# Kernel tuning notes

Hardware: AMD Instinct MI355X
Metric: run time of the kernel (lower is better)

## Reference

```python
import jax, jax.numpy as jnp
import numpy as np

K = 1024       # num_embeddings
D = 64         # embedding_dim
DECAY = 0.99
COMMIT = 0.25
EPS = 1e-05


def setup_inputs() -> dict:
    key = jax.random.key(0)
    k1, k2, k3 = jax.random.split(key, 3)
    x = jax.random.normal(k1, (16, 64, 64, 64), jnp.float32)  # NCHW, C == D
    embedding_weight = jax.random.normal(k2, (K, D), jnp.float32)
    ema_weight = jax.random.normal(k3, (K, D), jnp.float32)
    ema_cluster_size = jnp.zeros((K,), jnp.float32)
    return {"x": x, "embedding_weight": embedding_weight,
            "ema_cluster_size": ema_cluster_size, "ema_weight": ema_weight}


def reference(x, embedding_weight, ema_cluster_size, ema_weight):
    # NCHW -> NHWC, flatten tokens
    xp = jnp.transpose(x, (0, 2, 3, 1))            # [B,H,W,D]
    flat = xp.reshape(-1, D)                        # [N,D]
    dists = ((flat ** 2).sum(1, keepdims=True)
             + (embedding_weight ** 2).sum(1)
             - 2.0 * flat @ embedding_weight.T)     # [N,K]
    idx = jnp.argmin(dists, axis=1)                 # [N]
    encodings = jax.nn.one_hot(idx, K, dtype=flat.dtype)  # [N,K]
    quantized = jnp.take(embedding_weight, idx, axis=0).reshape(xp.shape)
    # training-mode EMA updates (scatter-add instead of dense one-hot matmuls)
    counts = jnp.zeros((K,), flat.dtype).at[idx].add(1.0)
    new_cs = ema_cluster_size * DECAY + (1.0 - DECAY) * counts
    n = new_cs.sum()
    new_cs = (new_cs + EPS) / (n + K * EPS) * n     # Laplace smoothing
    dw = jnp.zeros((K, D), flat.dtype).at[idx].add(flat)
    new_ema_weight = ema_weight * DECAY + (1.0 - DECAY) * dw
    new_embedding = new_ema_weight / new_cs[:, None]
    # commitment loss and straight-through estimator
    e_latent_loss = jnp.mean((jax.lax.stop_gradient(quantized) - xp) ** 2)
    loss = COMMIT * e_latent_loss
    q_st = xp + jax.lax.stop_gradient(quantized - xp)
    return (loss, jnp.transpose(q_st, (0, 3, 1, 2)), encodings,
            new_embedding, new_cs, new_ema_weight)
```

## Files before the change

kernel.cpp:

```cpp
#include <hip/hip_runtime.h>

#define HW 4096
#define DECAYF 0.99f
#define ONEMF 0.01f
#define EPSF 1e-5f
#define BIAS 192.0f

typedef __bf16 bf16x8 __attribute__((ext_vector_type(8)));
typedef float f32x4 __attribute__((ext_vector_type(4)));
typedef unsigned short ushort8 __attribute__((ext_vector_type(8)));

#define WS_DW     0
#define WS_COUNTS 1048576
#define WS_NCHALF 1064960
#define WS_SSE    1065984
#define WS_IDX    1066000
#define WS_EHI    1131536
#define WS_ELO    1164304

__device__ __forceinline__ float wave_reduce_add(float v) {
#pragma unroll
    for (int o = 32; o > 0; o >>= 1) v += __shfl_xor(v, o, 64);
    return v;
}

__device__ __forceinline__ unsigned short bf_rne(float f) {
    unsigned int u = __float_as_uint(f);
    unsigned int r = u + 0x7fffu + ((u >> 16) & 1u);
    return (unsigned short)(r >> 16);
}

__device__ __forceinline__ unsigned med3u(unsigned a, unsigned b, unsigned c) {
    unsigned mn = a < b ? a : b;
    unsigned mx = a > b ? a : b;
    unsigned t = mx < c ? mx : c;
    return mn > t ? mn : t;
}

__global__ __launch_bounds__(256) void prep_kernel(const float* __restrict__ E,
                                                   float* __restrict__ ws) {
    const int bid = blockIdx.x, tid = threadIdx.x;
    const int id = bid * 256 + tid;
    ws[id] = 0.0f;
    if (bid == 0 && tid == 0) ws[WS_SSE] = 0.0f;
    if (bid < 256) {
        const float v = E[id];
        const unsigned short h = bf_rne(v);
        const float hf = __uint_as_float((unsigned int)h << 16);
        const unsigned short l = bf_rne(v - hf);
        ((unsigned short*)(ws + WS_EHI))[id] = h;
        ((unsigned short*)(ws + WS_ELO))[id] = l;
        const float s = wave_reduce_add(v * v);
        if ((tid & 63) == 0) ws[WS_NCHALF + (id >> 6)] = -0.5f * s;
    }
}

__global__ __launch_bounds__(256) void vq_main(const float* __restrict__ x,
                                               const float* __restrict__ E,
                                               float* __restrict__ out,
                                               float* __restrict__ ws) {
    const int tid = threadIdx.x;
    const int lane = tid & 63;
    const int w = tid >> 6;
    const int q = lane >> 4, m = lane & 15;
    const int blk = blockIdx.x;
    const int bb = blk >> 5;
    const int hw0 = (blk & 31) << 7;
    const int tok0 = blk << 7;

    __shared__ float xs[128 * 68];
    __shared__ unsigned t1s[4][32][16], t2s[4][32][16];
    __shared__ int idx_sh[128];

    {
        const float* xb = x + ((size_t)bb << 18) + hw0;
#pragma unroll
        for (int cc = 0; cc < 32; ++cc) {
            const int id = cc * 256 + tid;
            const int c = id >> 7, t = id & 127;
            xs[t * 68 + c] = xb[((size_t)c << 12) + t];
        }
    }
    __syncthreads();

    bf16x8 Ah[2][2], Al[2][2];
#pragma unroll
    for (int t = 0; t < 2; ++t) {
        const int tok = w * 32 + t * 16 + m;
#pragma unroll
        for (int s = 0; s < 2; ++s) {
            const float* p = &xs[tok * 68 + s * 32 + q * 8];
            ushort8 hu, lu;
#pragma unroll
            for (int j = 0; j < 8; ++j) {
                const float f = p[j];
                const unsigned short h = bf_rne(f);
                const float hf = __uint_as_float((unsigned int)h << 16);
                hu[j] = h;
                lu[j] = bf_rne(f - hf);
            }
            Ah[t][s] = __builtin_bit_cast(bf16x8, hu);
            Al[t][s] = __builtin_bit_cast(bf16x8, lu);
        }
    }

    const ushort8* __restrict__ Ehp = (const ushort8*)(ws + WS_EHI);
    const ushort8* __restrict__ Elp = (const ushort8*)(ws + WS_ELO);
    const float* __restrict__ ncp = ws + WS_NCHALF;

    unsigned b1[2][4] = {{0,0,0,0},{0,0,0,0}}, b2[2][4] = {{0,0,0,0},{0,0,0,0}};

    ushort8 nb0h = Ehp[m * 8 + q];
    ushort8 nb1h = Ehp[m * 8 + 4 + q];
    ushort8 nb0l = Elp[m * 8 + q];
    ushort8 nb1l = Elp[m * 8 + 4 + q];
    float nnc = ncp[m];

    for (int ck = 0; ck < 64; ++ck) {
        const ushort8 c0h = nb0h, c1h = nb1h, c0l = nb0l, c1l = nb1l;
        const float nc = nnc;
        if (ck < 63) {
            const int code = (ck + 1) * 16 + m;
            nb0h = Ehp[code * 8 + q];
            nb1h = Ehp[code * 8 + 4 + q];
            nb0l = Elp[code * 8 + q];
            nb1l = Elp[code * 8 + 4 + q];
            nnc = ncp[code];
        }
        const bf16x8 bh0 = __builtin_bit_cast(bf16x8, c0h);
        const bf16x8 bh1 = __builtin_bit_cast(bf16x8, c1h);
        const bf16x8 bl0 = __builtin_bit_cast(bf16x8, c0l);
        const bf16x8 bl1 = __builtin_bit_cast(bf16x8, c1l);
        const float base = nc + BIAS;
#pragma unroll
        for (int t = 0; t < 2; ++t) {
            f32x4 acc = {base, base, base, base};
            acc = __builtin_amdgcn_mfma_f32_16x16x32_bf16(Ah[t][0], bh0, acc, 0, 0, 0);
            acc = __builtin_amdgcn_mfma_f32_16x16x32_bf16(Ah[t][1], bh1, acc, 0, 0, 0);
            acc = __builtin_amdgcn_mfma_f32_16x16x32_bf16(Al[t][0], bh0, acc, 0, 0, 0);
            acc = __builtin_amdgcn_mfma_f32_16x16x32_bf16(Al[t][1], bh1, acc, 0, 0, 0);
            acc = __builtin_amdgcn_mfma_f32_16x16x32_bf16(Ah[t][0], bl0, acc, 0, 0, 0);
            acc = __builtin_amdgcn_mfma_f32_16x16x32_bf16(Ah[t][1], bl1, acc, 0, 0, 0);
#pragma unroll
            for (int r = 0; r < 4; ++r) {
                const unsigned p = (__float_as_uint(acc[r]) & ~63u) | (unsigned)ck;
                b2[t][r] = med3u(b1[t][r], b2[t][r], p);
                b1[t][r] = b1[t][r] > p ? b1[t][r] : p;
            }
        }
    }

#pragma unroll
    for (int t = 0; t < 2; ++t)
#pragma unroll
        for (int r = 0; r < 4; ++r) {
            t1s[w][t * 16 + q * 4 + r][m] = b1[t][r];
            t2s[w][t * 16 + q * 4 + r][m] = b2[t][r];
        }

    float dval = 0.0f;
    if (lane < 32) {
        unsigned s1 = 0, s2 = 0;
        int c1 = 0, c2 = 0;
#pragma unroll 4
        for (int mm = 0; mm < 16; ++mm) {
            const unsigned a = t1s[w][lane][mm];
            const int codeA = (int)((a & 63u) << 4) | mm;
            if (a > s1) { s2 = s1; c2 = c1; s1 = a; c1 = codeA; }
            else if (a > s2) { s2 = a; c2 = codeA; }
            const unsigned bsec = t2s[w][lane][mm];
            if (bsec > s2) { s2 = bsec; c2 = (int)((bsec & 63u) << 4) | mm; }
        }
        const int tokL = w * 32 + lane;
        const int ca = c1 < c2 ? c1 : c2;
        const int cb = c1 < c2 ? c2 : c1;
        const f32x4* Ea4 = (const f32x4*)(E + ca * 64);
        const f32x4* Eb4 = (const f32x4*)(E + cb * 64);
        const f32x4* xr4 = (const f32x4*)(&xs[tokL * 68]);
        double sa = 0, ea = 0, sb = 0, eb = 0, x2 = 0;
#pragma unroll 4
        for (int c4 = 0; c4 < 16; ++c4) {
            const f32x4 ev = Ea4[c4], fv = Eb4[c4], xv4 = xr4[c4];
#pragma unroll
            for (int j = 0; j < 4; ++j) {
                const double xv = (double)xv4[j];
                const double va = (double)ev[j], vb = (double)fv[j];
                sa += xv * va; ea += va * va;
                sb += xv * vb; eb += vb * vb;
                x2 += xv * xv;
            }
        }
        const double qa = ea - 2.0 * sa;
        const double qb = eb - 2.0 * sb;
        int best; double qq;
        if (qb < qa) { best = cb; qq = qb; } else { best = ca; qq = qa; }
        idx_sh[tokL] = best;
        ((int*)(ws + WS_IDX))[tok0 + tokL] = best;
        float dd = (float)(qq + x2);
        dval = dd < 0.f ? 0.f : dd;
        atomicAdd(&ws[WS_COUNTS + (blk & 15) * 1024 + best], 1.0f);
    }
    const float ssum = wave_reduce_add(dval);
    if (lane == 0) atomicAdd(&ws[WS_SSE], ssum);
    __syncthreads();

    float* outq = out + 1;
#pragma unroll
    for (int cc = 0; cc < 32; ++cc) {
        const int id = cc * 256 + tid;
        const int c = id >> 7, t = id & 127;
        const int kb = idx_sh[t];
        const float xv = xs[t * 68 + c];
        const float eq = E[kb * 64 + c];
        outq[((size_t)(bb * 64 + c) << 12) + hw0 + t] = xv + (eq - xv);
    }
    {
        float* dwr = ws + WS_DW + (size_t)(blk & 15) * 65536;
#pragma unroll 4
        for (int tt = 0; tt < 32; ++tt) {
            const int t = w * 32 + tt;
            const int kb = idx_sh[t];
            atomicAdd(&dwr[kb * 64 + lane], xs[t * 68 + lane]);
        }
    }
}

__global__ __launch_bounds__(256) void enc_write(const float* __restrict__ ws,
                                                 float* __restrict__ out) {
    const int tid = threadIdx.x;
    const int c0 = tid << 2;
    const int row0 = blockIdx.x << 5;
    const int* __restrict__ idxp = (const int*)(ws + WS_IDX);
    float* enc = out + 1 + (size_t)4194304;
    for (int r = 0; r < 32; ++r) {
        const int row = row0 + r;
        const int kb = idxp[row];
        f32x4 v;
        v[0] = (c0 == kb) ? 1.0f : 0.0f;
        v[1] = (c0 + 1 == kb) ? 1.0f : 0.0f;
        v[2] = (c0 + 2 == kb) ? 1.0f : 0.0f;
        v[3] = (c0 + 3 == kb) ? 1.0f : 0.0f;
        *(f32x4*)(enc + (size_t)row * 1024 + c0) = v;
    }
}

__global__ __launch_bounds__(1024) void fin_cs(const float* __restrict__ cs_in,
                                               float* __restrict__ out,
                                               const float* __restrict__ ws) {
    __shared__ float red[16];
    __shared__ float n_sh;
    const int tid = threadIdx.x;
    float cnt = 0.f;
#pragma unroll
    for (int p = 0; p < 16; ++p) cnt += ws[WS_COUNTS + p * 1024 + tid];
    const float raw = cs_in[tid] * DECAYF + ONEMF * cnt;
    const float s = wave_reduce_add(raw);
    if ((tid & 63) == 0) red[tid >> 6] = s;
    __syncthreads();
    if (tid == 0) {
        float n = 0.f;
#pragma unroll
        for (int i = 0; i < 16; ++i) n += red[i];
        n_sh = n;
        out[0] = 0.25f * ws[WS_SSE] * (1.0f / 4194304.0f);
    }
    __syncthreads();
    const float n = n_sh;
    out[71368705 + tid] = (raw + EPSF) / (n + 1024.0f * EPSF) * n;
}

__global__ __launch_bounds__(256) void fin_w(const float* __restrict__ emaw,
                                             float* __restrict__ out,
                                             const float* __restrict__ ws) {
    const int i = blockIdx.x * 256 + threadIdx.x;
    float acc = 0.f;
#pragma unroll
    for (int p = 0; p < 16; ++p) acc += ws[WS_DW + p * 65536 + i];
    const float val = emaw[i] * DECAYF + ONEMF * acc;
    out[71369729 + i] = val;
    const float cs = out[71368705 + (i >> 6)];
    out[71303169 + i] = val / cs;
}

extern "C" void kernel_launch(void* const* d_in, const int* in_sizes, int n_in,
                              void* d_out, int out_size, void* d_ws, size_t ws_size,
                              hipStream_t stream) {
    const float* x    = (const float*)d_in[0];
    const float* E    = (const float*)d_in[1];
    const float* cs   = (const float*)d_in[2];
    const float* emaw = (const float*)d_in[3];
    float* out = (float*)d_out;
    float* ws  = (float*)d_ws;

    prep_kernel<<<4160, 256, 0, stream>>>(E, ws);
    vq_main<<<512, 256, 0, stream>>>(x, E, out, ws);
    enc_write<<<2048, 256, 0, stream>>>(ws, out);
    fin_cs<<<1, 1024, 0, stream>>>(cs, out, ws);
    fin_w<<<256, 256, 0, stream>>>(emaw, out, ws);
}
```

Before: 422.9 us.

## Split codebook scan across two wave groups and reduce top-2 via shuffles

Doubles the vq_main block to 512 threads so each token tile's codebook scan is split between two halves of 32 code chunks each. The inner loop now keeps two prefetch streams in flight. The per-lane top-2 merge is moved into cross-lane shuffles before the shared-memory exchange. This aims to double the waves per CU on a 512-block grid, which otherwise underfills the GPU, and to shorten the serial scan. The cost is more registers, extra shuffle and shared-memory traffic, and a final merge done by only half the waves.

New measurement: 419.0 us. No clear change (-0.9%).

```diff
diff --git a/kernel.cpp b/kernel.cpp
--- a/kernel.cpp
+++ b/kernel.cpp
@@ -55,13 +55,15 @@
     }
 }
 
-__global__ __launch_bounds__(256) void vq_main(const float* __restrict__ x,
-                                               const float* __restrict__ E,
-                                               float* __restrict__ out,
-                                               float* __restrict__ ws) {
+__global__ __launch_bounds__(512, 4) void vq_main(const float* __restrict__ x,
+                                                  const float* __restrict__ E,
+                                                  float* __restrict__ out,
+                                                  float* __restrict__ ws) {
     const int tid = threadIdx.x;
     const int lane = tid & 63;
     const int w = tid >> 6;
+    const int wg = w & 3;
+    const int kh = w >> 2;
     const int q = lane >> 4, m = lane & 15;
     const int blk = blockIdx.x;
     const int bb = blk >> 5;
@@ -69,14 +71,15 @@
     const int tok0 = blk << 7;
 
     __shared__ float xs[128 * 68];
-    __shared__ unsigned t1s[4][32][16], t2s[4][32][16];
+    __shared__ unsigned t1s[8][32][4], t2s[8][32][4];
+    __shared__ int t1c[8][32][4], t2c[8][32][4];
     __shared__ int idx_sh[128];
 
     {
         const float* xb = x + ((size_t)bb << 18) + hw0;
 #pragma unroll
-        for (int cc = 0; cc < 32; ++cc) {
-            const int id = cc * 256 + tid;
+        for (int cc = 0; cc < 16; ++cc) {
+            const int id = cc * 512 + tid;
             const int c = id >> 7, t = id & 127;
             xs[t * 68 + c] = xb[((size_t)c << 12) + t];
         }
@@ -86,7 +89,7 @@
     bf16x8 Ah[2][2], Al[2][2];
 #pragma unroll
     for (int t = 0; t < 2; ++t) {
-        const int tok = w * 32 + t * 16 + m;
+        const int tok = wg * 32 + t * 16 + m;
 #pragma unroll
         for (int s = 0; s < 2; ++s) {
             const float* p = &xs[tok * 68 + s * 32 + q * 8];
@@ -110,27 +113,21 @@
 
     unsigned b1[2][4] = {{0,0,0,0},{0,0,0,0}}, b2[2][4] = {{0,0,0,0},{0,0,0,0}};
 
-    ushort8 nb0h = Ehp[m * 8 + q];
-    ushort8 nb1h = Ehp[m * 8 + 4 + q];
-    ushort8 nb0l = Elp[m * 8 + q];
-    ushort8 nb1l = Elp[m * 8 + 4 + q];
-    float nnc = ncp[m];
-
-    for (int ck = 0; ck < 64; ++ck) {
-        const ushort8 c0h = nb0h, c1h = nb1h, c0l = nb0l, c1l = nb1l;
-        const float nc = nnc;
-        if (ck < 63) {
-            const int code = (ck + 1) * 16 + m;
-            nb0h = Ehp[code * 8 + q];
-            nb1h = Ehp[code * 8 + 4 + q];
-            nb0l = Elp[code * 8 + q];
-            nb1l = Elp[code * 8 + 4 + q];
-            nnc = ncp[code];
-        }
-        const bf16x8 bh0 = __builtin_bit_cast(bf16x8, c0h);
-        const bf16x8 bh1 = __builtin_bit_cast(bf16x8, c1h);
-        const bf16x8 bl0 = __builtin_bit_cast(bf16x8, c0l);
-        const bf16x8 bl1 = __builtin_bit_cast(bf16x8, c1l);
+    const int ck0 = kh * 32;
+    const int codeA0 = ck0 * 16 + m, codeB0 = (ck0 + 1) * 16 + m;
+    ushort8 hA0 = Ehp[codeA0 * 8 + q],     hA1 = Ehp[codeA0 * 8 + 4 + q];
+    ushort8 lA0 = Elp[codeA0 * 8 + q],     lA1 = Elp[codeA0 * 8 + 4 + q];
+    float   ncA = ncp[codeA0];
+    ushort8 hB0 = Ehp[codeB0 * 8 + q],     hB1 = Ehp[codeB0 * 8 + 4 + q];
+    ushort8 lB0 = Elp[codeB0 * 8 + q],     lB1 = Elp[codeB0 * 8 + 4 + q];
+    float   ncB = ncp[codeB0];
+
+    auto compute = [&](const ushort8& h0, const ushort8& h1, const ushort8& l0,
+                       const ushort8& l1, float nc, int ckv) {
+        const bf16x8 bh0 = __builtin_bit_cast(bf16x8, h0);
+        const bf16x8 bh1 = __builtin_bit_cast(bf16x8, h1);
+        const bf16x8 bl0 = __builtin_bit_cast(bf16x8, l0);
+        const bf16x8 bl1 = __builtin_bit_cast(bf16x8, l1);
         const float base = nc + BIAS;
 #pragma unroll
         for (int t = 0; t < 2; ++t) {
@@ -143,71 +140,129 @@
             acc = __builtin_amdgcn_mfma_f32_16x16x32_bf16(Ah[t][1], bl1, acc, 0, 0, 0);
 #pragma unroll
             for (int r = 0; r < 4; ++r) {
-                const unsigned p = (__float_as_uint(acc[r]) & ~63u) | (unsigned)ck;
+                const unsigned p = (__float_as_uint(acc[r]) & ~63u) | (unsigned)ckv;
                 b2[t][r] = med3u(b1[t][r], b2[t][r], p);
                 b1[t][r] = b1[t][r] > p ? b1[t][r] : p;
             }
         }
-    }
-
+    };
+
+    for (int j2 = 0; j2 < 16; ++j2) {
+        const int ckA = ck0 + 2 * j2;
+        const ushort8 ch0 = hA0, ch1 = hA1, cl0 = lA0, cl1 = lA1; const float cnc = ncA;
+        {
+            const int nc_ = (j2 < 15) ? (ckA + 2) * 16 + m : codeA0;
+            hA0 = Ehp[nc_ * 8 + q]; hA1 = Ehp[nc_ * 8 + 4 + q];
+            lA0 = Elp[nc_ * 8 + q]; lA1 = Elp[nc_ * 8 + 4 + q];
+            ncA = ncp[nc_];
+        }
+        compute(ch0, ch1, cl0, cl1, cnc, ckA);
+        const ushort8 dh0 = hB0, dh1 = hB1, dl0 = lB0, dl1 = lB1; const float dnc = ncB;
+        {
+            const int nc_ = (j2 < 15) ? (ckA + 3) * 16 + m : codeB0;
+            hB0 = Ehp[nc_ * 8 + q]; hB1 = Ehp[nc_ * 8 + 4 + q];
+            lB0 = Elp[nc_ * 8 + q]; lB1 = Elp[nc_ * 8 + 4 + q];
+            ncB = ncp[nc_];
+        }
+        compute(dh0, dh1, dl0, dl1, dnc, ckA + 1);
+    }
+
+    int c1[2][4], c2[2][4];
 #pragma unroll
     for (int t = 0; t < 2; ++t)
 #pragma unroll
         for (int r = 0; r < 4; ++r) {
-            t1s[w][t * 16 + q * 4 + r][m] = b1[t][r];
-            t2s[w][t * 16 + q * 4 + r][m] = b2[t][r];
-        }
+            c1[t][r] = (int)((b1[t][r] & 63u) << 4) | m;
+            c2[t][r] = (int)((b2[t][r] & 63u) << 4) | m;
+        }
+#pragma unroll
+    for (int d = 1; d < 4; d <<= 1) {
+#pragma unroll
+        for (int t = 0; t < 2; ++t)
+#pragma unroll
+            for (int r = 0; r < 4; ++r) {
+                const unsigned o1 = __shfl_xor(b1[t][r], d, 64);
+                const int      oc1 = __shfl_xor(c1[t][r], d, 64);
+                const unsigned o2 = __shfl_xor(b2[t][r], d, 64);
+                const int      oc2 = __shfl_xor(c2[t][r], d, 64);
+                const bool win = o1 > b1[t][r];
+                const unsigned n1 = win ? o1 : b1[t][r]; const int nc1 = win ? oc1 : c1[t][r];
+                const unsigned ls = win ? b1[t][r] : o1; const int lc = win ? c1[t][r] : oc1;
+                const unsigned os = win ? o2 : b2[t][r]; const int oc = win ? oc2 : c2[t][r];
+                const bool sec = ls > os;
+                b1[t][r] = n1; c1[t][r] = nc1;
+                b2[t][r] = sec ? ls : os; c2[t][r] = sec ? lc : oc;
+            }
+    }
+    if ((m & 3) == 0) {
+        const int g = m >> 2;
+#pragma unroll
+        for (int t = 0; t < 2; ++t)
+#pragma unroll
+            for (int r = 0; r < 4; ++r) {
+                const int trow = t * 16 + q * 4 + r;
+                t1s[w][trow][g] = b1[t][r]; t1c[w][trow][g] = c1[t][r];
+                t2s[w][trow][g] = b2[t][r]; t2c[w][trow][g] = c2[t][r];
+            }
+    }
+    __syncthreads();
 
     float dval = 0.0f;
-    if (lane < 32) {
-        unsigned s1 = 0, s2 = 0;
-        int c1 = 0, c2 = 0;
+    if (w < 4) {
+        if (lane < 32) {
+            const int trow = lane;
+            unsigned s1 = 0, s2 = 0;
+            int cc1 = 0, cc2 = 0;
+#pragma unroll
+            for (int h = 0; h < 2; ++h) {
+                const int ww = wg + h * 4;
+#pragma unroll
+                for (int g = 0; g < 4; ++g) {
+                    const unsigned a = t1s[ww][trow][g]; const int ac = t1c[ww][trow][g];
+                    if (a > s1) { s2 = s1; cc2 = cc1; s1 = a; cc1 = ac; }
+                    else if (a > s2) { s2 = a; cc2 = ac; }
+                    const unsigned bs = t2s[ww][trow][g]; const int bc = t2c[ww][trow][g];
+                    if (bs > s2) { s2 = bs; cc2 = bc; }
+                }
+            }
+            const int tokL = wg * 32 + lane;
+            const int ca = cc1 < cc2 ? cc1 : cc2;
+            const int cb = cc1 < cc2 ? cc2 : cc1;
+            const f32x4* Ea4 = (const f32x4*)(E + ca * 64);
+            const f32x4* Eb4 = (const f32x4*)(E + cb * 64);
+            const f32x4* xr4 = (const f32x4*)(&xs[tokL * 68]);
+            double sa = 0, ea = 0, sb = 0, eb = 0, x2 = 0;
 #pragma unroll 4
-        for (int mm = 0; mm < 16; ++mm) {
-            const unsigned a = t1s[w][lane][mm];
-            const int codeA = (int)((a & 63u) << 4) | mm;
-            if (a > s1) { s2 = s1; c2 = c1; s1 = a; c1 = codeA; }
-            else if (a > s2) { s2 = a; c2 = codeA; }
-            const unsigned bsec = t2s[w][lane][mm];
-            if (bsec > s2) { s2 = bsec; c2 = (int)((bsec & 63u) << 4) | mm; }
-        }
-        const int tokL = w * 32 + lane;
-        const int ca = c1 < c2 ? c1 : c2;
-        const int cb = c1 < c2 ? c2 : c1;
-        const f32x4* Ea4 = (const f32x4*)(E + ca * 64);
-        const f32x4* Eb4 = (const f32x4*)(E + cb * 64);
-        const f32x4* xr4 = (const f32x4*)(&xs[tokL * 68]);
-        double sa = 0, ea = 0, sb = 0, eb = 0, x2 = 0;
-#pragma unroll 4
-        for (int c4 = 0; c4 < 16; ++c4) {
-            const f32x4 ev = Ea4[c4], fv = Eb4[c4], xv4 = xr4[c4];
-#pragma unroll
-            for (int j = 0; j < 4; ++j) {
-                const double xv = (double)xv4[j];
-                const double va = (double)ev[j], vb = (double)fv[j];
-                sa += xv * va; ea += va * va;
-                sb += xv * vb; eb += vb * vb;
-                x2 += xv * xv;
-            }
-        }
-        const double qa = ea - 2.0 * sa;
-        const double qb = eb - 2.0 * sb;
-        int best; double qq;
-        if (qb < qa) { best = cb; qq = qb; } else { best = ca; qq = qa; }
-        idx_sh[tokL] = best;
-        ((int*)(ws + WS_IDX))[tok0 + tokL] = best;
-        float dd = (float)(qq + x2);
-        dval = dd < 0.f ? 0.f : dd;
-        atomicAdd(&ws[WS_COUNTS + (blk & 15) * 1024 + best], 1.0f);
-    }
-    const float ssum = wave_reduce_add(dval);
-    if (lane == 0) atomicAdd(&ws[WS_SSE], ssum);
+            for (int c4 = 0; c4 < 16; ++c4) {
+                const f32x4 ev = Ea4[c4], fv = Eb4[c4], xv4 = xr4[c4];
+#pragma unroll
+                for (int j = 0; j < 4; ++j) {
+                    const double xv = (double)xv4[j];
+                    const double va = (double)ev[j], vb = (double)fv[j];
+                    sa += xv * va; ea += va * va;
+                    sb += xv * vb; eb += vb * vb;
+                    x2 += xv * xv;
+                }
+            }
+            const double qa = ea - 2.0 * sa;
+            const double qb = eb - 2.0 * sb;
+            int best; double qq;
+            if (qb < qa) { best = cb; qq = qb; } else { best = ca; qq = qa; }
+            idx_sh[tokL] = best;
+            ((int*)(ws + WS_IDX))[tok0 + tokL] = best;
+            float dd = (float)(qq + x2);
+            dval = dd < 0.f ? 0.f : dd;
+            atomicAdd(&ws[WS_COUNTS + (blk & 15) * 1024 + best], 1.0f);
+        }
+        const float ssum = wave_reduce_add(dval);
+        if (lane == 0) atomicAdd(&ws[WS_SSE], ssum);
+    }
     __syncthreads();
 
     float* outq = out + 1;
 #pragma unroll
-    for (int cc = 0; cc < 32; ++cc) {
-        const int id = cc * 256 + tid;
+    for (int cc = 0; cc < 16; ++cc) {
+        const int id = cc * 512 + tid;
         const int c = id >> 7, t = id & 127;
         const int kb = idx_sh[t];
         const float xv = xs[t * 68 + c];
@@ -217,8 +272,8 @@
     {
         float* dwr = ws + WS_DW + (size_t)(blk & 15) * 65536;
 #pragma unroll 4
-        for (int tt = 0; tt < 32; ++tt) {
-            const int t = w * 32 + tt;
+        for (int tt = 0; tt < 16; ++tt) {
+            const int t = w * 16 + tt;
             const int kb = idx_sh[t];
             atomicAdd(&dwr[kb * 64 + lane], xs[t * 68 + lane]);
         }
@@ -293,7 +348,7 @@
     float* ws  = (float*)d_ws;
 
     prep_kernel<<<4160, 256, 0, stream>>>(E, ws);
-    vq_main<<<512, 256, 0, stream>>>(x, E, out, ws);
+    vq_main<<<512, 512, 0, stream>>>(x, E, out, ws);
     enc_write<<<2048, 256, 0, stream>>>(ws, out);
     fin_cs<<<1, 1024, 0, stream>>>(cs, out, ws);
     fin_w<<<256, 256, 0, stream>>>(emaw, out, ws);
```

## Split VQ search into codebook-panel kernel, top-2 merge, and output pass

Applied to the files above, without the earlier changes.

The single 512-block search kernel becomes a 4096-block kernel where each block handles 128 tokens against a 128-code panel, staged in LDS. Each block writes per-panel top-2 candidates to workspace, and a separate merge kernel picks the final index with a double-precision recheck. The quantized output and dw scatter move into their own kernel, and workspace zeroing uses hipMemsetAsync. The intent is more parallelism and occupancy across the device, paid for with extra launches, extra global traffic for top-2 candidates, and re-reading x several times.

Result: slower. 439.6 us (+3.9%).

```diff
diff --git a/kernel.cpp b/kernel.cpp
--- a/kernel.cpp
+++ b/kernel.cpp
@@ -1,10 +1,8 @@
 #include <hip/hip_runtime.h>
 
-#define HW 4096
 #define DECAYF 0.99f
 #define ONEMF 0.01f
 #define EPSF 1e-5f
-#define BIAS 192.0f
 
 typedef __bf16 bf16x8 __attribute__((ext_vector_type(8)));
 typedef float f32x4 __attribute__((ext_vector_type(4)));
@@ -17,6 +15,7 @@
 #define WS_IDX    1066000
 #define WS_EHI    1131536
 #define WS_ELO    1164304
+#define WS_TOP2   1197072
 
 __device__ __forceinline__ float wave_reduce_add(float v) {
 #pragma unroll
@@ -30,198 +29,247 @@
     return (unsigned short)(r >> 16);
 }
 
-__device__ __forceinline__ unsigned med3u(unsigned a, unsigned b, unsigned c) {
-    unsigned mn = a < b ? a : b;
-    unsigned mx = a > b ? a : b;
-    unsigned t = mx < c ? mx : c;
-    return mn > t ? mn : t;
-}
-
 __global__ __launch_bounds__(256) void prep_kernel(const float* __restrict__ E,
                                                    float* __restrict__ ws) {
-    const int bid = blockIdx.x, tid = threadIdx.x;
-    const int id = bid * 256 + tid;
-    ws[id] = 0.0f;
-    if (bid == 0 && tid == 0) ws[WS_SSE] = 0.0f;
-    if (bid < 256) {
-        const float v = E[id];
-        const unsigned short h = bf_rne(v);
-        const float hf = __uint_as_float((unsigned int)h << 16);
-        const unsigned short l = bf_rne(v - hf);
-        ((unsigned short*)(ws + WS_EHI))[id] = h;
-        ((unsigned short*)(ws + WS_ELO))[id] = l;
-        const float s = wave_reduce_add(v * v);
-        if ((tid & 63) == 0) ws[WS_NCHALF + (id >> 6)] = -0.5f * s;
-    }
-}
-
-__global__ __launch_bounds__(256) void vq_main(const float* __restrict__ x,
-                                               const float* __restrict__ E,
-                                               float* __restrict__ out,
-                                               float* __restrict__ ws) {
+    const int id = blockIdx.x * 256 + threadIdx.x;
+    const float v = E[id];
+    const unsigned short h = bf_rne(v);
+    const float hf = __uint_as_float((unsigned int)h << 16);
+    const unsigned short l = bf_rne(v - hf);
+    ((unsigned short*)(ws + WS_EHI))[id] = h;
+    ((unsigned short*)(ws + WS_ELO))[id] = l;
+    const float s = wave_reduce_add(v * v);
+    if ((threadIdx.x & 63) == 0) ws[WS_NCHALF + (id >> 6)] = -0.5f * s;
+}
+
+__global__ __launch_bounds__(256, 2) void vq_panel(const float* __restrict__ x,
+                                                   float* __restrict__ ws) {
     const int tid = threadIdx.x;
     const int lane = tid & 63;
     const int w = tid >> 6;
     const int q = lane >> 4, m = lane & 15;
+    const int bx = blockIdx.x;
+    const int tb = bx >> 3;
+    const int pb = bx & 7;
+    const int bb = tb >> 5;
+    const int hw0 = (tb & 31) << 7;
+    const int tok0 = tb << 7;
+    const int k0 = pb << 7;
+
+    __shared__ __align__(16) unsigned short Ash[128 * 72];
+    __shared__ __align__(16) unsigned short Asl[128 * 72];
+    __shared__ __align__(16) unsigned short Bsh[128 * 72];
+    __shared__ __align__(16) unsigned short Bsl[128 * 72];
+
+    {
+        const ushort8* __restrict__ Eh = (const ushort8*)(ws + WS_EHI);
+        const ushort8* __restrict__ El = (const ushort8*)(ws + WS_ELO);
+#pragma unroll
+        for (int i = 0; i < 4; ++i) {
+            const int idx = i * 256 + tid;
+            const int row = idx >> 3, ch = idx & 7;
+            *(ushort8*)&Bsh[row * 72 + ch * 8] = Eh[(k0 + row) * 8 + ch];
+            *(ushort8*)&Bsl[row * 72 + ch * 8] = El[(k0 + row) * 8 + ch];
+        }
+    }
+    {
+        const float* xb = x + ((size_t)bb << 18) + hw0;
+#pragma unroll
+        for (int i = 0; i < 32; ++i) {
+            const int idx = i * 256 + tid;
+            const int c = idx >> 7, t = idx & 127;
+            const float f = xb[((size_t)c << 12) + t];
+            const unsigned short h = bf_rne(f);
+            const float hf = __uint_as_float((unsigned int)h << 16);
+            Ash[t * 72 + c] = h;
+            Asl[t * 72 + c] = bf_rne(f - hf);
+        }
+    }
+    __syncthreads();
+
+    bf16x8 Ah[2][2], Al[2][2];
+#pragma unroll
+    for (int t2 = 0; t2 < 2; ++t2) {
+        const int tok = w * 32 + t2 * 16 + m;
+#pragma unroll
+        for (int s = 0; s < 2; ++s) {
+            Ah[t2][s] = __builtin_bit_cast(bf16x8, *(const ushort8*)&Ash[tok * 72 + s * 32 + q * 8]);
+            Al[t2][s] = __builtin_bit_cast(bf16x8, *(const ushort8*)&Asl[tok * 72 + s * 32 + q * 8]);
+        }
+    }
+
+    const float* __restrict__ ncp = ws + WS_NCHALF + k0;
+
+    float s1[2][4], s2[2][4];
+    int i1[2][4], i2[2][4];
+#pragma unroll
+    for (int t2 = 0; t2 < 2; ++t2)
+#pragma unroll
+        for (int r = 0; r < 4; ++r) { s1[t2][r] = -1e30f; s2[t2][r] = -1e30f; i1[t2][r] = 0; i2[t2][r] = 0; }
+
+#pragma unroll 2
+    for (int ct = 0; ct < 8; ++ct) {
+        const int crow = ct * 16 + m;
+        const bf16x8 Bh0 = __builtin_bit_cast(bf16x8, *(const ushort8*)&Bsh[crow * 72 + q * 8]);
+        const bf16x8 Bh1 = __builtin_bit_cast(bf16x8, *(const ushort8*)&Bsh[crow * 72 + 32 + q * 8]);
+        const bf16x8 Bl0 = __builtin_bit_cast(bf16x8, *(const ushort8*)&Bsl[crow * 72 + q * 8]);
+        const bf16x8 Bl1 = __builtin_bit_cast(bf16x8, *(const ushort8*)&Bsl[crow * 72 + 32 + q * 8]);
+        const float base = ncp[crow];
+        const int code = k0 + crow;
+#pragma unroll
+        for (int t2 = 0; t2 < 2; ++t2) {
+            f32x4 acc = {base, base, base, base};
+            acc = __builtin_amdgcn_mfma_f32_16x16x32_bf16(Ah[t2][0], Bh0, acc, 0, 0, 0);
+            acc = __builtin_amdgcn_mfma_f32_16x16x32_bf16(Ah[t2][1], Bh1, acc, 0, 0, 0);
+            acc = __builtin_amdgcn_mfma_f32_16x16x32_bf16(Al[t2][0], Bh0, acc, 0, 0, 0);
+            acc = __builtin_amdgcn_mfma_f32_16x16x32_bf16(Al[t2][1], Bh1, acc, 0, 0, 0);
+            acc = __builtin_amdgcn_mfma_f32_16x16x32_bf16(Ah[t2][0], Bl0, acc, 0, 0, 0);
+            acc = __builtin_amdgcn_mfma_f32_16x16x32_bf16(Ah[t2][1], Bl1, acc, 0, 0, 0);
+#pragma unroll
+            for (int r = 0; r < 4; ++r) {
+                const float sc = acc[r];
+                const bool cA = sc > s1[t2][r];
+                const bool cB = sc > s2[t2][r];
+                s2[t2][r] = cA ? s1[t2][r] : (cB ? sc : s2[t2][r]);
+                i2[t2][r] = cA ? i1[t2][r] : (cB ? code : i2[t2][r]);
+                s1[t2][r] = cA ? sc : s1[t2][r];
+                i1[t2][r] = cA ? code : i1[t2][r];
+            }
+        }
+    }
+
+#pragma unroll
+    for (int d = 1; d < 16; d <<= 1) {
+#pragma unroll
+        for (int t2 = 0; t2 < 2; ++t2)
+#pragma unroll
+            for (int r = 0; r < 4; ++r) {
+                const float o1 = __shfl_xor(s1[t2][r], d, 64);
+                const int   oc1 = __shfl_xor(i1[t2][r], d, 64);
+                const float o2 = __shfl_xor(s2[t2][r], d, 64);
+                const int   oc2 = __shfl_xor(i2[t2][r], d, 64);
+                const bool win = o1 > s1[t2][r];
+                const float n1 = win ? o1 : s1[t2][r]; const int nc1 = win ? oc1 : i1[t2][r];
+                const float ls = win ? s1[t2][r] : o1; const int lc = win ? i1[t2][r] : oc1;
+                const float os = win ? o2 : s2[t2][r]; const int oc = win ? oc2 : i2[t2][r];
+                const bool sec = ls > os;
+                s1[t2][r] = n1; i1[t2][r] = nc1;
+                s2[t2][r] = sec ? ls : os; i2[t2][r] = sec ? lc : oc;
+            }
+    }
+    if (m == 0) {
+        float* tp = ws + WS_TOP2;
+#pragma unroll
+        for (int t2 = 0; t2 < 2; ++t2)
+#pragma unroll
+            for (int r = 0; r < 4; ++r) {
+                const int tokL = w * 32 + t2 * 16 + q * 4 + r;
+                f32x4 v;
+                v[0] = s1[t2][r]; v[1] = __int_as_float(i1[t2][r]);
+                v[2] = s2[t2][r]; v[3] = __int_as_float(i2[t2][r]);
+                *(f32x4*)&tp[((size_t)(tok0 + tokL) * 8 + pb) * 4] = v;
+            }
+    }
+}
+
+__global__ __launch_bounds__(256) void vq_merge(const float* __restrict__ x,
+                                                const float* __restrict__ E,
+                                                float* __restrict__ ws) {
+    const int tid = threadIdx.x;
+    const int token = blockIdx.x * 256 + tid;
+    const f32x4* tp = (const f32x4*)(ws + WS_TOP2 + (size_t)token * 32);
+    float s1 = -1e30f, s2 = -1e30f;
+    int c1 = 0, c2 = 1;
+#pragma unroll
+    for (int p = 0; p < 8; ++p) {
+        const f32x4 v = tp[p];
+        const float a = v[0]; const int ac = __float_as_int(v[1]);
+        const float b = v[2]; const int bc = __float_as_int(v[3]);
+        if (a > s1) { s2 = s1; c2 = c1; s1 = a; c1 = ac; }
+        else if (a > s2) { s2 = a; c2 = ac; }
+        if (b > s2) { s2 = b; c2 = bc; }
+    }
+    const int ca = c1 < c2 ? c1 : c2;
+    const int cb = c1 < c2 ? c2 : c1;
+    const int bb = token >> 12;
+    const int hw = token & 4095;
+    const float* xb = x + ((size_t)bb << 18) + hw;
+    const f32x4* Ea4 = (const f32x4*)(E + ca * 64);
+    const f32x4* Eb4 = (const f32x4*)(E + cb * 64);
+    double sa = 0, ea = 0, sb = 0, eb = 0, x2 = 0;
+#pragma unroll 4
+    for (int c4 = 0; c4 < 16; ++c4) {
+        const f32x4 ev = Ea4[c4], fv = Eb4[c4];
+#pragma unroll
+        for (int j = 0; j < 4; ++j) {
+            const double xv = (double)xb[(size_t)(c4 * 4 + j) << 12];
+            const double va = (double)ev[j], vb = (double)fv[j];
+            sa += xv * va; ea += va * va;
+            sb += xv * vb; eb += vb * vb;
+            x2 += xv * xv;
+        }
+    }
+    const double qa = ea - 2.0 * sa;
+    const double qb = eb - 2.0 * sb;
+    int best; double qq;
+    if (qb < qa) { best = cb; qq = qb; } else { best = ca; qq = qa; }
+    ((int*)(ws + WS_IDX))[token] = best;
+    float dd = (float)(qq + x2);
+    if (dd < 0.f) dd = 0.f;
+    atomicAdd(&ws[WS_COUNTS + (blockIdx.x & 15) * 1024 + best], 1.0f);
+    const float ssum = wave_reduce_add(dd);
+    __shared__ float red[4];
+    if ((tid & 63) == 0) red[tid >> 6] = ssum;
+    __syncthreads();
+    if (tid == 0) atomicAdd(&ws[WS_SSE], red[0] + red[1] + red[2] + red[3]);
+}
+
+__global__ __launch_bounds__(256) void qst_dw(const float* __restrict__ x,
+                                              const float* __restrict__ E,
+                                              float* __restrict__ out,
+                                              float* __restrict__ ws) {
+    const int tid = threadIdx.x;
+    const int lane = tid & 63;
+    const int w = tid >> 6;
     const int blk = blockIdx.x;
     const int bb = blk >> 5;
     const int hw0 = (blk & 31) << 7;
     const int tok0 = blk << 7;
 
-    __shared__ float xs[128 * 68];
-    __shared__ unsigned t1s[4][32][16], t2s[4][32][16];
+    __shared__ float xs[128 * 65];
+    __shared__ float qs[128 * 65];
     __shared__ int idx_sh[128];
 
+    if (tid < 128) idx_sh[tid] = ((const int*)(ws + WS_IDX))[tok0 + tid];
     {
         const float* xb = x + ((size_t)bb << 18) + hw0;
 #pragma unroll
         for (int cc = 0; cc < 32; ++cc) {
             const int id = cc * 256 + tid;
             const int c = id >> 7, t = id & 127;
-            xs[t * 68 + c] = xb[((size_t)c << 12) + t];
-        }
-    }
-    __syncthreads();
-
-    bf16x8 Ah[2][2], Al[2][2];
-#pragma unroll
-    for (int t = 0; t < 2; ++t) {
-        const int tok = w * 32 + t * 16 + m;
-#pragma unroll
-        for (int s = 0; s < 2; ++s) {
-            const float* p = &xs[tok * 68 + s * 32 + q * 8];
-            ushort8 hu, lu;
-#pragma unroll
-            for (int j = 0; j < 8; ++j) {
-                const float f = p[j];
-                const unsigned short h = bf_rne(f);
-                const float hf = __uint_as_float((unsigned int)h << 16);
-                hu[j] = h;
-                lu[j] = bf_rne(f - hf);
-            }
-            Ah[t][s] = __builtin_bit_cast(bf16x8, hu);
-            Al[t][s] = __builtin_bit_cast(bf16x8, lu);
-        }
-    }
-
-    const ushort8* __restrict__ Ehp = (const ushort8*)(ws + WS_EHI);
-    const ushort8* __restrict__ Elp = (const ushort8*)(ws + WS_ELO);
-    const float* __restrict__ ncp = ws + WS_NCHALF;
-
-    unsigned b1[2][4] = {{0,0,0,0},{0,0,0,0}}, b2[2][4] = {{0,0,0,0},{0,0,0,0}};
-
-    ushort8 nb0h = Ehp[m * 8 + q];
-    ushort8 nb1h = Ehp[m * 8 + 4 + q];
-    ushort8 nb0l = Elp[m * 8 + q];
-    ushort8 nb1l = Elp[m * 8 + 4 + q];
-    float nnc = ncp[m];
-
-    for (int ck = 0; ck < 64; ++ck) {
-        const ushort8 c0h = nb0h, c1h = nb1h, c0l = nb0l, c1l = nb1l;
-        const float nc = nnc;
-        if (ck < 63) {
-            const int code = (ck + 1) * 16 + m;
-            nb0h = Ehp[code * 8 + q];
-            nb1h = Ehp[code * 8 + 4 + q];
-            nb0l = Elp[code * 8 + q];
-            nb1l = Elp[code * 8 + 4 + q];
-            nnc = ncp[code];
-        }
-        const bf16x8 bh0 = __builtin_bit_cast(bf16x8, c0h);
-        const bf16x8 bh1 = __builtin_bit_cast(bf16x8, c1h);
-        const bf16x8 bl0 = __builtin_bit_cast(bf16x8, c0l);
-        const bf16x8 bl1 = __builtin_bit_cast(bf16x8, c1l);
-        const float base = nc + BIAS;
-#pragma unroll
-        for (int t = 0; t < 2; ++t) {
-            f32x4 acc = {base, base, base, base};
-            acc = __builtin_amdgcn_mfma_f32_16x16x32_bf16(Ah[t][0], bh0, acc, 0, 0, 0);
-            acc = __builtin_amdgcn_mfma_f32_16x16x32_bf16(Ah[t][1], bh1, acc, 0, 0, 0);
-            acc = __builtin_amdgcn_mfma_f32_16x16x32_bf16(Al[t][0], bh0, acc, 0, 0, 0);
-            acc = __builtin_amdgcn_mfma_f32_16x16x32_bf16(Al[t][1], bh1, acc, 0, 0, 0);
-            acc = __builtin_amdgcn_mfma_f32_16x16x32_bf16(Ah[t][0], bl0, acc, 0, 0, 0);
-            acc = __builtin_amdgcn_mfma_f32_16x16x32_bf16(Ah[t][1], bl1, acc, 0, 0, 0);
-#pragma unroll
-            for (int r = 0; r < 4; ++r) {
-                const unsigned p = (__float_as_uint(acc[r]) & ~63u) | (unsigned)ck;
-                b2[t][r] = med3u(b1[t][r], b2[t][r], p);
-                b1[t][r] = b1[t][r] > p ? b1[t][r] : p;
-            }
-        }
-    }
-
-#pragma unroll
-    for (int t = 0; t < 2; ++t)
-#pragma unroll
-        for (int r = 0; r < 4; ++r) {
-            t1s[w][t * 16 + q * 4 + r][m] = b1[t][r];
-            t2s[w][t * 16 + q * 4 + r][m] = b2[t][r];
-        }
-
-    float dval = 0.0f;
-    if (lane < 32) {
-        unsigned s1 = 0, s2 = 0;
-        int c1 = 0, c2 = 0;
-#pragma unroll 4
-        for (int mm = 0; mm < 16; ++mm) {
-            const unsigned a = t1s[w][lane][mm];
-            const int codeA = (int)((a & 63u) << 4) | mm;
-            if (a > s1) { s2 = s1; c2 = c1; s1 = a; c1 = codeA; }
-            else if (a > s2) { s2 = a; c2 = codeA; }
-            const unsigned bsec = t2s[w][lane][mm];
-            if (bsec > s2) { s2 = bsec; c2 = (int)((bsec & 63u) << 4) | mm; }
-        }
-        const int tokL = w * 32 + lane;
-        const int ca = c1 < c2 ? c1 : c2;
-        const int cb = c1 < c2 ? c2 : c1;
-        const f32x4* Ea4 = (const f32x4*)(E + ca * 64);
-        const f32x4* Eb4 = (const f32x4*)(E + cb * 64);
-        const f32x4* xr4 = (const f32x4*)(&xs[tokL * 68]);
-        double sa = 0, ea = 0, sb = 0, eb = 0, x2 = 0;
-#pragma unroll 4
-        for (int c4 = 0; c4 < 16; ++c4) {
-            const f32x4 ev = Ea4[c4], fv = Eb4[c4], xv4 = xr4[c4];
-#pragma unroll
-            for (int j = 0; j < 4; ++j) {
-                const double xv = (double)xv4[j];
-                const double va = (double)ev[j], vb = (double)fv[j];
-                sa += xv * va; ea += va * va;
-                sb += xv * vb; eb += vb * vb;
-                x2 += xv * xv;
-            }
-        }
-        const double qa = ea - 2.0 * sa;
-        const double qb = eb - 2.0 * sb;
-        int best; double qq;
-        if (qb < qa) { best = cb; qq = qb; } else { best = ca; qq = qa; }
-        idx_sh[tokL] = best;
-        ((int*)(ws + WS_IDX))[tok0 + tokL] = best;
-        float dd = (float)(qq + x2);
-        dval = dd < 0.f ? 0.f : dd;
-        atomicAdd(&ws[WS_COUNTS + (blk & 15) * 1024 + best], 1.0f);
-    }
-    const float ssum = wave_reduce_add(dval);
-    if (lane == 0) atomicAdd(&ws[WS_SSE], ssum);
-    __syncthreads();
-
-    float* outq = out + 1;
-#pragma unroll
-    for (int cc = 0; cc < 32; ++cc) {
-        const int id = cc * 256 + tid;
-        const int c = id >> 7, t = id & 127;
-        const int kb = idx_sh[t];
-        const float xv = xs[t * 68 + c];
-        const float eq = E[kb * 64 + c];
-        outq[((size_t)(bb * 64 + c) << 12) + hw0 + t] = xv + (eq - xv);
-    }
+            xs[t * 65 + c] = xb[((size_t)c << 12) + t];
+        }
+    }
+    __syncthreads();
     {
         float* dwr = ws + WS_DW + (size_t)(blk & 15) * 65536;
 #pragma unroll 4
         for (int tt = 0; tt < 32; ++tt) {
             const int t = w * 32 + tt;
             const int kb = idx_sh[t];
-            atomicAdd(&dwr[kb * 64 + lane], xs[t * 68 + lane]);
-        }
+            qs[t * 65 + lane] = E[kb * 64 + lane];
+            atomicAdd(&dwr[kb * 64 + lane], xs[t * 65 + lane]);
+        }
+    }
+    __syncthreads();
+    float* outq = out + 1;
+#pragma unroll
+    for (int cc = 0; cc < 32; ++cc) {
+        const int id = cc * 256 + tid;
+        const int c = id >> 7, t = id & 127;
+        const float xv = xs[t * 65 + c];
+        const float eq = qs[t * 65 + c];
+        outq[((size_t)(bb * 64 + c) << 12) + hw0 + t] = xv + (eq - xv);
     }
 }
 
@@ -292,8 +340,11 @@
     float* out = (float*)d_out;
     float* ws  = (float*)d_ws;
 
-    prep_kernel<<<4160, 256, 0, stream>>>(E, ws);
-    vq_main<<<512, 256, 0, stream>>>(x, E, out, ws);
+    hipMemsetAsync(ws, 0, (size_t)(WS_SSE + 1) * sizeof(float), stream);
+    prep_kernel<<<256, 256, 0, stream>>>(E, ws);
+    vq_panel<<<4096, 256, 0, stream>>>(x, ws);
+    vq_merge<<<256, 256, 0, stream>>>(x, E, ws);
+    qst_dw<<<512, 256, 0, stream>>>(x, E, out, ws);
     enc_write<<<2048, 256, 0, stream>>>(ws, out);
     fin_cs<<<1, 1024, 0, stream>>>(cs, out, ws);
     fin_w<<<256, 256, 0, stream>>>(emaw, out, ws);
```
